# Performance work log

Hardware: AMD Instinct MI355X
Metric: run time of the kernel (lower is better)

Reference implementation:

```python
import jax, jax.numpy as jnp
import numpy as np

ALPHA = 0.2          # LeakyReLU negative slope
NEG_BIG = -9e15      # mask fill value from the original code
N, IN_F, OUT_F = 8192, 128, 64


def setup_inputs() -> dict:
    key = jax.random.key(0)
    k1, k2, k3, k4 = jax.random.split(key, 4)
    h = jax.random.normal(k1, (N, IN_F), dtype=jnp.float32)
    adj = jax.random.randint(k2, (N, N), 0, 2, dtype=jnp.int32)
    W = jax.random.normal(k3, (IN_F, OUT_F), dtype=jnp.float32) * 0.1
    a = jax.random.normal(k4, (2 * OUT_F, 1), dtype=jnp.float32) * 0.1
    return {"h": h, "adj": adj, "W": W, "a": a}


def reference(h, adj, W, a):
    # Wh: [N, F]
    Wh = h @ W
    # e_ij = leakyrelu([Wh_i ; Wh_j] . a) = leakyrelu(Wh_i.a1 + Wh_j.a2)
    # (identical math to the original NxNx2F concat, without materializing it)
    a1 = a[:OUT_F, 0]   # [F]
    a2 = a[OUT_F:, 0]   # [F]
    s1 = Wh @ a1        # [N]
    s2 = Wh @ a2        # [N]
    e = jax.nn.leaky_relu(s1[:, None] + s2[None, :], negative_slope=ALPHA)  # [N, N]
    e = jnp.where(adj > 0, e, jnp.float32(NEG_BIG))
    attention = jax.nn.softmax(e, axis=1)
    # dropout is identity at inference (training=False)
    h_prime = attention @ Wh  # [N, F]
    return jax.nn.elu(h_prime)  # concat=True -> elu
```

## Files before the change

### kernel.cpp

```cpp
#include <hip/hip_runtime.h>
#include <hip/hip_bf16.h>

#define N 8192
#define IN_F 128
#define OUT_F 64
#define LRELU_ALPHA 0.2f
#define PAD 520

typedef __attribute__((ext_vector_type(8))) short short8;
typedef __attribute__((ext_vector_type(4))) float float4v;
typedef __attribute__((ext_vector_type(4))) unsigned short ushortx4;

__device__ __forceinline__ unsigned short bf16_bits(float x) {
  unsigned u = __builtin_bit_cast(unsigned, x);
  u += 0x7fffu + ((u >> 16) & 1u);
  return (unsigned short)(u >> 16);
}

__global__ __launch_bounds__(256) void prep_kernel(
    const float* __restrict__ h, const float* __restrict__ W,
    const float* __restrict__ a, float* __restrict__ s1,
    float* __restrict__ s2, unsigned short* __restrict__ whT) {
  const int tid = threadIdx.x;
  const int row = blockIdx.x * 4 + (tid >> 6);
  const int k = tid & 63;
  const float* hr = h + row * IN_F;
  float acc = 0.f;
#pragma unroll 8
  for (int c = 0; c < IN_F; ++c) acc = fmaf(hr[c], W[c * OUT_F + k], acc);
  whT[(long)k * N + row] = bf16_bits(acc);
  float p1 = acc * a[k];
  float p2 = acc * a[OUT_F + k];
#pragma unroll
  for (int off = 32; off > 0; off >>= 1) {
    p1 += __shfl_xor(p1, off);
    p2 += __shfl_xor(p2, off);
  }
  if (k == 0) { s1[row] = p1; s2[row] = p2; }
}

__global__ __launch_bounds__(256) void repack_kernel(
    const unsigned short* __restrict__ whT, unsigned short* __restrict__ whF) {
  const int f = blockIdx.x * 256 + threadIdx.x;
  const int lane = f & 63, tt = (f >> 6) & 3, c = f >> 8;
  const int r16 = lane & 15, quad = lane >> 4;
  const short8 v = *(const short8*)(whT + (long)(tt * 16 + r16) * N + c * 32 + quad * 8);
  *(short8*)(whF + (long)f * 8) = v;
}

__device__ __forceinline__ void p_write(unsigned short* pr, int c, int4 av,
                                        float4 s2v, float s1w) {
  float e0 = s1w + s2v.x; e0 = fmaxf(e0, LRELU_ALPHA * e0);
  float e1 = s1w + s2v.y; e1 = fmaxf(e1, LRELU_ALPHA * e1);
  float e2 = s1w + s2v.z; e2 = fmaxf(e2, LRELU_ALPHA * e2);
  float e3 = s1w + s2v.w; e3 = fmaxf(e3, LRELU_ALPHA * e3);
  const float p0 = av.x > 0 ? __expf(e0) : 0.f;
  const float p1 = av.y > 0 ? __expf(e1) : 0.f;
  const float p2 = av.z > 0 ? __expf(e2) : 0.f;
  const float p3 = av.w > 0 ? __expf(e3) : 0.f;
  ushortx4 pk = {bf16_bits(p0), bf16_bits(p1), bf16_bits(p2), bf16_bits(p3)};
  *(ushortx4*)(pr + c) = pk;
}

__global__ __launch_bounds__(1024, 4) void gat_kernel(
    const int* __restrict__ adj, const float* __restrict__ s1,
    const float* __restrict__ s2, const unsigned short* __restrict__ whF,
    float* __restrict__ out) {
  __shared__ __align__(16) unsigned short pbuf[2][16][PAD];
  const int tid = threadIdx.x;
  const int w = tid >> 6, L = tid & 63;
  const int r16 = L & 15, quad = L >> 4;
  const int row0 = blockIdx.x * 16;
  const long arow = (long)(row0 + w) * N;
  const float s1w = s1[row0 + w];

  float4v acc0 = {0.f, 0.f, 0.f, 0.f};
  float4v acc1 = {0.f, 0.f, 0.f, 0.f};
  float4v acc2 = {0.f, 0.f, 0.f, 0.f};
  float4v acc3 = {0.f, 0.f, 0.f, 0.f};
  float4v accD = {0.f, 0.f, 0.f, 0.f};
  const short ONE = (short)0x3F80;
  const short8 ones = {ONE, ONE, ONE, ONE, ONE, ONE, ONE, ONE};

  {
    const int c = L * 4;
    const int4 a0 = *(const int4*)(adj + arow + c);
    const int4 a1 = *(const int4*)(adj + arow + 256 + c);
    const float4 sv0 = *(const float4*)(s2 + c);
    const float4 sv1 = *(const float4*)(s2 + 256 + c);
    p_write(pbuf[0][w], c, a0, sv0, s1w);
    p_write(pbuf[0][w], 256 + c, a1, sv1, s1w);
  }
  __syncthreads();

  for (int it = 0; it < 16; ++it) {
    const int b = it & 1;
    int4 na0, na1;
    float4 ns0, ns1;
    if (it < 15) {
      const long base = arow + (it + 1) * 512 + L * 4;
      na0 = *(const int4*)(adj + base);
      na1 = *(const int4*)(adj + base + 256);
      ns0 = *(const float4*)(s2 + (it + 1) * 512 + L * 4);
      ns1 = *(const float4*)(s2 + (it + 1) * 512 + 256 + L * 4);
    }
    const int c32 = it * 16 + w;
    const short8 afrag = *(const short8*)(&pbuf[b][r16][w * 32 + quad * 8]);
    const unsigned short* bp = whF + ((long)c32 * 256 + L) * 8;
    const short8 b0 = *(const short8*)(bp);
    const short8 b1 = *(const short8*)(bp + 512);
    const short8 b2 = *(const short8*)(bp + 1024);
    const short8 b3 = *(const short8*)(bp + 1536);
    acc0 = __builtin_amdgcn_mfma_f32_16x16x32_bf16(afrag, b0, acc0, 0, 0, 0);
    acc1 = __builtin_amdgcn_mfma_f32_16x16x32_bf16(afrag, b1, acc1, 0, 0, 0);
    acc2 = __builtin_amdgcn_mfma_f32_16x16x32_bf16(afrag, b2, acc2, 0, 0, 0);
    acc3 = __builtin_amdgcn_mfma_f32_16x16x32_bf16(afrag, b3, acc3, 0, 0, 0);
    accD = __builtin_amdgcn_mfma_f32_16x16x32_bf16(afrag, ones, accD, 0, 0, 0);
    if (it < 15) {
      unsigned short* pr = pbuf[b ^ 1][w];
      const int c = L * 4;
      p_write(pr, c, na0, ns0, s1w);
      p_write(pr, 256 + c, na1, ns1, s1w);
    }
    __syncthreads();
  }

  float* M = (float*)pbuf;
  if (w >= 8) {
    float* S = M + (w - 8) * 1040;
#pragma unroll
    for (int reg = 0; reg < 4; ++reg) {
      const int r = quad * 4 + reg;
      S[r * 64 + 0 * 16 + r16] = acc0[reg];
      S[r * 64 + 1 * 16 + r16] = acc1[reg];
      S[r * 64 + 2 * 16 + r16] = acc2[reg];
      S[r * 64 + 3 * 16 + r16] = acc3[reg];
      if (r16 == 0) S[1024 + r] = accD[reg];
    }
  }
  __syncthreads();
  if (w < 8) {
    float* S = M + w * 1040;
#pragma unroll
    for (int reg = 0; reg < 4; ++reg) {
      const int r = quad * 4 + reg;
      S[r * 64 + 0 * 16 + r16] += acc0[reg];
      S[r * 64 + 1 * 16 + r16] += acc1[reg];
      S[r * 64 + 2 * 16 + r16] += acc2[reg];
      S[r * 64 + 3 * 16 + r16] += acc3[reg];
      if (r16 == 0) S[1024 + r] += accD[reg];
    }
  }
  __syncthreads();
  {
    const int r = tid >> 6, k = tid & 63;
    float Sv = 0.f, Lv = 0.f;
#pragma unroll
    for (int s = 0; s < 8; ++s) {
      Sv += M[s * 1040 + r * 64 + k];
      Lv += M[s * 1040 + 1024 + r];
    }
    const float v = Sv / Lv;
    out[(long)(row0 + r) * OUT_F + k] = v > 0.f ? v : expm1f(v);
  }
}

extern "C" void kernel_launch(void* const* d_in, const int* in_sizes, int n_in,
                              void* d_out, int out_size, void* d_ws, size_t ws_size,
                              hipStream_t stream) {
  const float* h = (const float*)d_in[0];
  const int* adj = (const int*)d_in[1];
  const float* W = (const float*)d_in[2];
  const float* a = (const float*)d_in[3];
  float* out = (float*)d_out;

  float* s1 = (float*)d_ws;
  float* s2 = s1 + N;
  unsigned short* whT = (unsigned short*)(s2 + N);
  unsigned short* whF = whT + (long)OUT_F * N;

  prep_kernel<<<N / 4, 256, 0, stream>>>(h, W, a, s1, s2, whT);
  repack_kernel<<<N * OUT_F / 8 / 256, 256, 0, stream>>>(whT, whF);
  gat_kernel<<<N / 16, 1024, 0, stream>>>(adj, s1, s2, whF, out);
}
```

Measured before the change: 391.1 us.

## Double chunk size and prefetch adjacency two iterations ahead

Each loop iteration now covers 1024 columns instead of 512, which halves the number of iterations and block barriers. Adjacency and s2 loads are issued two chunks ahead and held in registers, so more global loads are in flight while the MFMA work runs. The P computation for the next buffer is also moved ahead of the MFMAs. The cost is a larger LDS buffer (about 66KB) and more registers, which may lower occupancy under the 1024-thread launch bound.

Result: no change. 397.6 us (+1.6%).

```diff
diff --git a/kernel.cpp b/kernel.cpp
--- a/kernel.cpp
+++ b/kernel.cpp
@@ -5,7 +5,9 @@
 #define IN_F 128
 #define OUT_F 64
 #define LRELU_ALPHA 0.2f
-#define PAD 520
+#define CH 1024
+#define NIT 8
+#define PSTR 1040
 
 typedef __attribute__((ext_vector_type(8))) short short8;
 typedef __attribute__((ext_vector_type(4))) float float4v;
@@ -66,7 +68,7 @@
     const int* __restrict__ adj, const float* __restrict__ s1,
     const float* __restrict__ s2, const unsigned short* __restrict__ whF,
     float* __restrict__ out) {
-  __shared__ __align__(16) unsigned short pbuf[2][16][PAD];
+  __shared__ __align__(16) unsigned short pbuf[2][16][PSTR];
   const int tid = threadIdx.x;
   const int w = tid >> 6, L = tid & 63;
   const int r16 = L & 15, quad = L >> 4;
@@ -82,45 +84,55 @@
   const short ONE = (short)0x3F80;
   const short8 ones = {ONE, ONE, ONE, ONE, ONE, ONE, ONE, ONE};
 
-  {
-    const int c = L * 4;
-    const int4 a0 = *(const int4*)(adj + arow + c);
-    const int4 a1 = *(const int4*)(adj + arow + 256 + c);
-    const float4 sv0 = *(const float4*)(s2 + c);
-    const float4 sv1 = *(const float4*)(s2 + 256 + c);
-    p_write(pbuf[0][w], c, a0, sv0, s1w);
-    p_write(pbuf[0][w], 256 + c, a1, sv1, s1w);
+  int4 ra[4];
+  float4 rs[4];
+#pragma unroll
+  for (int k = 0; k < 4; ++k) {
+    ra[k] = *(const int4*)(adj + arow + k * 256 + L * 4);
+    rs[k] = *(const float4*)(s2 + k * 256 + L * 4);
+  }
+#pragma unroll
+  for (int k = 0; k < 4; ++k)
+    p_write(pbuf[0][w], k * 256 + L * 4, ra[k], rs[k], s1w);
+#pragma unroll
+  for (int k = 0; k < 4; ++k) {
+    ra[k] = *(const int4*)(adj + arow + CH + k * 256 + L * 4);
+    rs[k] = *(const float4*)(s2 + CH + k * 256 + L * 4);
   }
   __syncthreads();
 
-  for (int it = 0; it < 16; ++it) {
+  for (int it = 0; it < NIT; ++it) {
     const int b = it & 1;
-    int4 na0, na1;
-    float4 ns0, ns1;
-    if (it < 15) {
-      const long base = arow + (it + 1) * 512 + L * 4;
-      na0 = *(const int4*)(adj + base);
-      na1 = *(const int4*)(adj + base + 256);
-      ns0 = *(const float4*)(s2 + (it + 1) * 512 + L * 4);
-      ns1 = *(const float4*)(s2 + (it + 1) * 512 + 256 + L * 4);
+    if (it < NIT - 1) {
+      unsigned short* pr = pbuf[b ^ 1][w];
+#pragma unroll
+      for (int k = 0; k < 4; ++k)
+        p_write(pr, k * 256 + L * 4, ra[k], rs[k], s1w);
+      if (it < NIT - 2) {
+        const long base = arow + (long)(it + 2) * CH + L * 4;
+        const int sbase = (it + 2) * CH + L * 4;
+#pragma unroll
+        for (int k = 0; k < 4; ++k) {
+          ra[k] = *(const int4*)(adj + base + k * 256);
+          rs[k] = *(const float4*)(s2 + sbase + k * 256);
+        }
+      }
     }
-    const int c32 = it * 16 + w;
-    const short8 afrag = *(const short8*)(&pbuf[b][r16][w * 32 + quad * 8]);
-    const unsigned short* bp = whF + ((long)c32 * 256 + L) * 8;
-    const short8 b0 = *(const short8*)(bp);
-    const short8 b1 = *(const short8*)(bp + 512);
-    const short8 b2 = *(const short8*)(bp + 1024);
-    const short8 b3 = *(const short8*)(bp + 1536);
-    acc0 = __builtin_amdgcn_mfma_f32_16x16x32_bf16(afrag, b0, acc0, 0, 0, 0);
-    acc1 = __builtin_amdgcn_mfma_f32_16x16x32_bf16(afrag, b1, acc1, 0, 0, 0);
-    acc2 = __builtin_amdgcn_mfma_f32_16x16x32_bf16(afrag, b2, acc2, 0, 0, 0);
-    acc3 = __builtin_amdgcn_mfma_f32_16x16x32_bf16(afrag, b3, acc3, 0, 0, 0);
-    accD = __builtin_amdgcn_mfma_f32_16x16x32_bf16(afrag, ones, accD, 0, 0, 0);
-    if (it < 15) {
-      unsigned short* pr = pbuf[b ^ 1][w];
-      const int c = L * 4;
-      p_write(pr, c, na0, ns0, s1w);
-      p_write(pr, 256 + c, na1, ns1, s1w);
+#pragma unroll
+    for (int sub = 0; sub < 2; ++sub) {
+      const int lc = (sub * 16 + w) * 32;
+      const short8 afrag = *(const short8*)(&pbuf[b][r16][lc + quad * 8]);
+      const int c32 = it * 32 + sub * 16 + w;
+      const unsigned short* bp = whF + ((long)c32 * 256 + L) * 8;
+      const short8 b0 = *(const short8*)(bp);
+      const short8 b1 = *(const short8*)(bp + 512);
+      const short8 b2 = *(const short8*)(bp + 1024);
+      const short8 b3 = *(const short8*)(bp + 1536);
+      acc0 = __builtin_amdgcn_mfma_f32_16x16x32_bf16(afrag, b0, acc0, 0, 0, 0);
+      acc1 = __builtin_amdgcn_mfma_f32_16x16x32_bf16(afrag, b1, acc1, 0, 0, 0);
+      acc2 = __builtin_amdgcn_mfma_f32_16x16x32_bf16(afrag, b2, acc2, 0, 0, 0);
+      acc3 = __builtin_amdgcn_mfma_f32_16x16x32_bf16(afrag, b3, acc3, 0, 0, 0);
+      accD = __builtin_amdgcn_mfma_f32_16x16x32_bf16(afrag, ones, accD, 0, 0, 0);
     }
     __syncthreads();
   }
```
